# Kernel optimization log

Hardware: AMD Instinct MI355X
Metric: run time of the kernel (lower is better)

The kernel has to match this reference:

```python
import jax, jax.numpy as jnp
import numpy as np

DEGREE_X = 3
DEGREE_Y = 3
OUT_X = 1024
OUT_Y = 1024
DIM = 3
N_CTRL = 256
EPS = 1e-05


def _normalize_knots(k):
    # Module's knot normalization: clamp negatives to 1e-4, cumsum, rescale to [0, 1].
    k = jnp.where(k < 0.0, jnp.asarray(1e-4, k.dtype), k)
    k = jnp.cumsum(k)
    return (k - k[0]) / (k[-1] - k[0])


def _find_spans(u, knots, n_ctrl):
    # searchsorted(right=True) - 1, with the upper-boundary fixup from the module.
    spans = jnp.searchsorted(knots, u, side='right') - 1
    return jnp.where(u == knots[n_ctrl], n_ctrl - 1, spans)


def _basis(u, knots, span, degree):
    # Cox-de Boor recursion, vectorized over all evaluation points u (E,).
    # left[j] = u - U[span+1-j], right[j] = U[span+j] - u (standard recursion).
    K = knots.shape[0]
    cols = [jnp.ones_like(u)]
    left = [None]
    right = [None]
    for j in range(1, degree + 1):
        left.append(u - knots[jnp.mod(span + 1 - j, K)])
        right.append(knots[jnp.mod(span + j, K)] - u)
        saved = jnp.zeros_like(u)
        new_cols = []
        for r in range(j):
            temp = cols[r] / (right[r + 1] + left[j - r])
            new_cols.append(saved + right[r + 1] * temp)
            saved = left[j - r] * temp
        new_cols.append(saved)
        cols = new_cols
    return jnp.stack(cols, axis=-1)  # (E, degree+1)


def _surface(control_points, knot_vector_x, knot_vector_y):
    nx, ny = control_points.shape[0], control_points.shape[1]
    kx = _normalize_knots(knot_vector_x[0])  # (Kx,)
    ky = _normalize_knots(knot_vector_y[0])  # (Ky,)
    ex = jnp.linspace(EPS, 1.0 - EPS, OUT_X, dtype=control_points.dtype)
    ey = jnp.linspace(EPS, 1.0 - EPS, OUT_Y, dtype=control_points.dtype)
    sx = _find_spans(ex, kx, nx)  # (Ex,)
    sy = _find_spans(ey, ky, ny)  # (Ey,)
    bx = _basis(ex, kx, sx, DEGREE_X)  # (Ex, dx+1)
    by = _basis(ey, ky, sy, DEGREE_Y)  # (Ey, dy+1)
    # Local control-point footprint: indices span - degree + l, l = 0..degree.
    ix = jnp.mod(sx[None, :] - DEGREE_X + jnp.arange(DEGREE_X + 1)[:, None], nx)  # (dx+1, Ex)
    iy = jnp.mod(sy[None, :] - DEGREE_Y + jnp.arange(DEGREE_Y + 1)[:, None], ny)  # (dy+1, Ey)
    pts = control_points[ix[:, None, :, None], iy[None, :, None, :]]  # (dx+1, dy+1, Ex, Ey, 3)
    surf = jnp.einsum('el,fr,lrefd->efd', bx, by, pts)  # (Ex, Ey, 3)
    return surf[None, :, :, :DIM]  # (1, Ex, Ey, DIM)


def setup_inputs() -> dict:
    key = jax.random.key(0)
    k1, k2, k3 = jax.random.split(key, 3)
    control_points = jax.random.normal(k1, (N_CTRL, N_CTRL, 3), dtype=jnp.float32)
    knot_vector_x = jax.random.uniform(k2, (1, N_CTRL + DEGREE_X + 1), dtype=jnp.float32)
    knot_vector_y = jax.random.uniform(k3, (1, N_CTRL + DEGREE_Y + 1), dtype=jnp.float32)
    return {'control_points': control_points, 'knot_vector_x': knot_vector_x, 'knot_vector_y': knot_vector_y}


def reference(control_points, knot_vector_x, knot_vector_y):
    return _surface(control_points, knot_vector_x, knot_vector_y)
```

## Files before the change

### kernel.cpp

```cpp
#include <hip/hip_runtime.h>


#define KLEN  260
#define NCTRL 256
#define OUTN  1024
#define DEG   3
#define EPSV  1e-5
#define CHUNK 5

__device__ __forceinline__ void basis_eval(const float* __restrict__ k,
                                           int idx, float* w, int* ci) {
  const double step = (1.0 - 2.0 * (double)EPSV) / (double)(OUTN - 1);
  const float u = (float)((double)EPSV + (double)idx * step);

  int lo = 0, hi = KLEN;
  #pragma unroll
  for (int it = 0; it < 9; ++it) {
    int mid = (lo + hi) >> 1;
    bool c = (k[mid] <= u);
    lo = c ? mid + 1 : lo;
    hi = c ? hi  : mid;
  }
  int span = lo - 1;
  if (u == k[NCTRL]) span = NCTRL - 1;

  float left[DEG + 1], right[DEG + 1], cols[DEG + 1];
  cols[0] = 1.f;
  #pragma unroll
  for (int j = 1; j <= DEG; ++j) {
    int li = span + 1 - j; if (li < 0)     li += KLEN;
    int ri = span + j;     if (ri >= KLEN) ri -= KLEN;
    left[j]  = u - k[li];
    right[j] = k[ri] - u;
    float saved = 0.f;
    #pragma unroll
    for (int r = 0; r < j; ++r) {
      float temp = cols[r] * __builtin_amdgcn_rcpf(right[r + 1] + left[j - r]);
      cols[r] = saved + right[r + 1] * temp;
      saved = left[j - r] * temp;
    }
    cols[j] = saved;
  }
  #pragma unroll
  for (int l = 0; l <= DEG; ++l) {
    w[l]  = cols[l];
    ci[l] = (span - DEG + l) & (NCTRL - 1);
  }
}

__global__ __launch_bounds__(256) void nurbs_fused(
    const float* __restrict__ cp,
    const float* __restrict__ kvx, const float* __restrict__ kvy,
    float* __restrict__ out) {
  __shared__ float kn[2][KLEN];
  __shared__ float sbuf[256 * 3];

  const int t    = threadIdx.x;
  const int wave = t >> 6;
  const int lane = t & 63;

  if (wave < 2) {
    const float* kv = (wave == 0) ? kvx : kvy;
    float v[CHUNK];
    float lsum = 0.f;
    if (lane < 52) {
      #pragma unroll
      for (int j = 0; j < CHUNK; ++j) {
        float x = kv[lane * CHUNK + j];
        x = (x < 0.f) ? 1e-4f : x;
        v[j] = x;
        lsum += x;
      }
    } else {
      #pragma unroll
      for (int j = 0; j < CHUNK; ++j) v[j] = 0.f;
    }
    float s = lsum;
    #pragma unroll
    for (int d = 1; d < 64; d <<= 1) {
      float n = __shfl_up(s, d);
      if (lane >= d) s += n;
    }
    const float excl  = s - lsum;
    const float total = __shfl(s, 51);
    const float c0    = __shfl(v[0], 0);
    const float inv_d = 1.f / (total - c0);
    if (lane < 52) {
      float run = excl;
      #pragma unroll
      for (int j = 0; j < CHUNK; ++j) {
        run += v[j];
        kn[wave][lane * CHUNK + j] = (run - c0) * inv_d;
      }
    }
  }
  __syncthreads();

  const int bx    = blockIdx.x;
  const int e     = bx >> 2;
  const int fbase = (bx & 3) << 8;
  const int f     = fbase + t;

  float wE[4], wF[4];
  int   iE[4], iF[4];
  basis_eval(kn[0], e, wE, iE);
  basis_eval(kn[1], f, wF, iF);

  float ax = 0.f, ay = 0.f, az = 0.f;
  #pragma unroll
  for (int l = 0; l < 4; ++l) {
    const float* rowp = cp + iE[l] * (NCTRL * 3);
    const float wl = wE[l];
    #pragma unroll
    for (int r = 0; r < 4; ++r) {
      const float w = wl * wF[r];
      const float* p = rowp + iF[r] * 3;
      ax = fmaf(w, p[0], ax);
      ay = fmaf(w, p[1], ay);
      az = fmaf(w, p[2], az);
    }
  }

  sbuf[t * 3 + 0] = ax;
  sbuf[t * 3 + 1] = ay;
  sbuf[t * 3 + 2] = az;
  __syncthreads();

  float4* ob = (float4*)(out + (size_t)(e * OUTN + fbase) * 3);
  if (t < 192) ob[t] = ((const float4*)sbuf)[t];
}

extern "C" void kernel_launch(void* const* d_in, const int* in_sizes, int n_in,
                              void* d_out, int out_size, void* d_ws, size_t ws_size,
                              hipStream_t stream) {
  (void)in_sizes; (void)n_in; (void)out_size; (void)d_ws; (void)ws_size;
  const float* cp  = (const float*)d_in[0];
  const float* kvx = (const float*)d_in[1];
  const float* kvy = (const float*)d_in[2];
  float* out = (float*)d_out;

  nurbs_fused<<<4096, 256, 0, stream>>>(cp, kvx, kvy, out);
}
```

Before: 73.68 us.

## Compute four output rows per block and reuse F-direction partial sums across rows

Each block now produces four consecutive e rows instead of one. The grid shrinks by four, so the knot normalization and the per-thread F basis evaluation are amortized over four rows. When the four e spans lie within a six-row window, each thread contracts six control-point rows with its F weights once and then combines them with padded E weights from shared memory. This cuts global gathers from 64 to 24 per four outputs. Otherwise it falls back to the direct per-row loop. The cost is more registers, more shared memory, fewer blocks, and a divergent fallback path.

```diff
diff --git a/kernel.cpp b/kernel.cpp
--- a/kernel.cpp
+++ b/kernel.cpp
@@ -7,23 +7,29 @@
 #define DEG   3
 #define EPSV  1e-5
 #define CHUNK 5
-
-__device__ __forceinline__ void basis_eval(const float* __restrict__ k,
-                                           int idx, float* w, int* ci) {
+#define WROWS 6
+
+__device__ __forceinline__ float uval(int idx) {
   const double step = (1.0 - 2.0 * (double)EPSV) / (double)(OUTN - 1);
-  const float u = (float)((double)EPSV + (double)idx * step);
-
+  return (float)((double)EPSV + (double)idx * step);
+}
+
+__device__ __forceinline__ int find_span(const float* __restrict__ k, float u) {
   int lo = 0, hi = KLEN;
   #pragma unroll
   for (int it = 0; it < 9; ++it) {
     int mid = (lo + hi) >> 1;
     bool c = (k[mid] <= u);
     lo = c ? mid + 1 : lo;
-    hi = c ? hi  : mid;
+    hi = c ? hi : mid;
   }
   int span = lo - 1;
   if (u == k[NCTRL]) span = NCTRL - 1;
-
+  return span;
+}
+
+__device__ __forceinline__ void basis_from_span(const float* __restrict__ k,
+                                                float u, int span, float* w) {
   float left[DEG + 1], right[DEG + 1], cols[DEG + 1];
   cols[0] = 1.f;
   #pragma unroll
@@ -42,10 +48,7 @@
     cols[j] = saved;
   }
   #pragma unroll
-  for (int l = 0; l <= DEG; ++l) {
-    w[l]  = cols[l];
-    ci[l] = (span - DEG + l) & (NCTRL - 1);
-  }
+  for (int l = 0; l <= DEG; ++l) w[l] = cols[l];
 }
 
 __global__ __launch_bounds__(256) void nurbs_fused(
@@ -53,7 +56,10 @@
     const float* __restrict__ kvx, const float* __restrict__ kvy,
     float* __restrict__ out) {
   __shared__ float kn[2][KLEN];
-  __shared__ float sbuf[256 * 3];
+  __shared__ float wEraw[4][4];
+  __shared__ int   sspan[4];
+  __shared__ float wEp[4][WROWS];
+  __shared__ float sbuf[4][256 * 3];
 
   const int t    = threadIdx.x;
   const int wave = t >> 6;
@@ -97,37 +103,104 @@
   __syncthreads();
 
   const int bx    = blockIdx.x;
-  const int e     = bx >> 2;
+  const int e0    = (bx >> 2) << 2;
   const int fbase = (bx & 3) << 8;
   const int f     = fbase + t;
 
-  float wE[4], wF[4];
-  int   iE[4], iF[4];
-  basis_eval(kn[0], e, wE, iE);
-  basis_eval(kn[1], f, wF, iF);
-
-  float ax = 0.f, ay = 0.f, az = 0.f;
-  #pragma unroll
-  for (int l = 0; l < 4; ++l) {
-    const float* rowp = cp + iE[l] * (NCTRL * 3);
-    const float wl = wE[l];
-    #pragma unroll
-    for (int r = 0; r < 4; ++r) {
-      const float w = wl * wF[r];
-      const float* p = rowp + iF[r] * 3;
-      ax = fmaf(w, p[0], ax);
-      ay = fmaf(w, p[1], ay);
-      az = fmaf(w, p[2], az);
-    }
-  }
-
-  sbuf[t * 3 + 0] = ax;
-  sbuf[t * 3 + 1] = ay;
-  sbuf[t * 3 + 2] = az;
-  __syncthreads();
-
-  float4* ob = (float4*)(out + (size_t)(e * OUTN + fbase) * 3);
-  if (t < 192) ob[t] = ((const float4*)sbuf)[t];
+  if (t < 4) {
+    const float ue = uval(e0 + t);
+    const int sp = find_span(kn[0], ue);
+    sspan[t] = sp;
+    float w4[4];
+    basis_from_span(kn[0], ue, sp, w4);
+    #pragma unroll
+    for (int l = 0; l < 4; ++l) wEraw[t][l] = w4[l];
+  }
+  __syncthreads();
+
+  if (t < 4 * WROWS) {
+    const int e = t / WROWS, i = t % WROWS;
+    const int d = sspan[e] - sspan[0];
+    const int l = i - d;
+    wEp[e][i] = ((unsigned)l < 4u) ? wEraw[e][l] : 0.f;
+  }
+
+  const float uf = uval(f);
+  const int spf = find_span(kn[1], uf);
+  float wF[4];
+  basis_from_span(kn[1], uf, spf, wF);
+  int iF[4];
+  #pragma unroll
+  for (int r = 0; r < 4; ++r) iF[r] = (spf - DEG + r) & (NCTRL - 1);
+
+  __syncthreads();
+
+  const int span0 = sspan[0];
+  const int sdiff = sspan[3] - span0;
+
+  float acc[4][3];
+  #pragma unroll
+  for (int e = 0; e < 4; ++e) {
+    acc[e][0] = 0.f; acc[e][1] = 0.f; acc[e][2] = 0.f;
+  }
+
+  if (sdiff <= WROWS - 4) {
+    #pragma unroll
+    for (int i = 0; i < WROWS; ++i) {
+      const int row = (span0 - DEG + i) & (NCTRL - 1);
+      const float* rowp = cp + row * (NCTRL * 3);
+      float rb0 = 0.f, rb1 = 0.f, rb2 = 0.f;
+      #pragma unroll
+      for (int r = 0; r < 4; ++r) {
+        const float* p = rowp + iF[r] * 3;
+        rb0 = fmaf(wF[r], p[0], rb0);
+        rb1 = fmaf(wF[r], p[1], rb1);
+        rb2 = fmaf(wF[r], p[2], rb2);
+      }
+      #pragma unroll
+      for (int e = 0; e < 4; ++e) {
+        const float we = wEp[e][i];
+        acc[e][0] = fmaf(we, rb0, acc[e][0]);
+        acc[e][1] = fmaf(we, rb1, acc[e][1]);
+        acc[e][2] = fmaf(we, rb2, acc[e][2]);
+      }
+    }
+  } else {
+    #pragma unroll
+    for (int e = 0; e < 4; ++e) {
+      const int spe = sspan[e];
+      #pragma unroll
+      for (int l = 0; l < 4; ++l) {
+        const int row = (spe - DEG + l) & (NCTRL - 1);
+        const float* rowp = cp + row * (NCTRL * 3);
+        const float wl = wEraw[e][l];
+        #pragma unroll
+        for (int r = 0; r < 4; ++r) {
+          const float w = wl * wF[r];
+          const float* p = rowp + iF[r] * 3;
+          acc[e][0] = fmaf(w, p[0], acc[e][0]);
+          acc[e][1] = fmaf(w, p[1], acc[e][1]);
+          acc[e][2] = fmaf(w, p[2], acc[e][2]);
+        }
+      }
+    }
+  }
+
+  #pragma unroll
+  for (int e = 0; e < 4; ++e) {
+    sbuf[e][t * 3 + 0] = acc[e][0];
+    sbuf[e][t * 3 + 1] = acc[e][1];
+    sbuf[e][t * 3 + 2] = acc[e][2];
+  }
+  __syncthreads();
+
+  #pragma unroll
+  for (int e = 0; e < 4; ++e) {
+    if (t < 192) {
+      float4* ob = (float4*)(out + (size_t)((e0 + e) * OUTN + fbase) * 3);
+      ob[t] = ((const float4*)sbuf[e])[t];
+    }
+  }
 }
 
 extern "C" void kernel_launch(void* const* d_in, const int* in_sizes, int n_in,
@@ -139,5 +212,5 @@
   const float* kvy = (const float*)d_in[2];
   float* out = (float*)d_out;
 
-  nurbs_fused<<<4096, 256, 0, stream>>>(cp, kvx, kvy, out);
-}
+  nurbs_fused<<<1024, 256, 0, stream>>>(cp, kvx, kvy, out);
+}
```

New measurement: 66.94 us. 1.1x faster.
